# Performance work log

Hardware: AMD Instinct MI355X
Metric: run time of the kernel (lower is better)

The kernel has to match this reference:

```python
import jax, jax.numpy as jnp
import numpy as np

S1, S2, S3 = 2, 16, 1  # hardcoded layer sizes from __init__


def _lstm_cell(x, h, c, w_ih, w_hh, b_ih, b_hh):
    # torch.nn.LSTMCell gate order: i, f, g, o
    gates = x @ w_ih.T + b_ih + h @ w_hh.T + b_hh
    i, f, g, o = jnp.split(gates, 4, axis=-1)
    i = jax.nn.sigmoid(i)
    f = jax.nn.sigmoid(f)
    g = jnp.tanh(g)
    o = jax.nn.sigmoid(o)
    c_new = f * c + i * g
    h_new = o * jnp.tanh(c_new)
    return h_new, c_new


def setup_inputs() -> dict:
    key = jax.random.key(0)
    ks = jax.random.split(key, 16)
    B, T = 16384, 2048
    x = jax.random.normal(ks[0], (B, T * S1), dtype=jnp.float32)

    def u(k, shape, fan):
        bound = 1.0 / np.sqrt(fan)
        return jax.random.uniform(k, shape, jnp.float32, -bound, bound)

    return {
        "x": x,
        # lstm1: LSTMCell(2, 2)
        "w_ih1": u(ks[1], (4 * S1, S1), S1), "w_hh1": u(ks[2], (4 * S1, S1), S1),
        "b_ih1": u(ks[3], (4 * S1,), S1),   "b_hh1": u(ks[4], (4 * S1,), S1),
        # lstm2: LSTMCell(2, 16)
        "w_ih2": u(ks[5], (4 * S2, S1), S2), "w_hh2": u(ks[6], (4 * S2, S2), S2),
        "b_ih2": u(ks[7], (4 * S2,), S2),   "b_hh2": u(ks[8], (4 * S2,), S2),
        # lstm3: LSTMCell(16, 1)
        "w_ih3": u(ks[9], (4 * S3, S2), S3), "w_hh3": u(ks[10], (4 * S3, S3), S3),
        "b_ih3": u(ks[11], (4 * S3,), S3),  "b_hh3": u(ks[12], (4 * S3,), S3),
        # linear: Linear(1, 1)
        "w_lin": u(ks[13], (S3, S3), S3), "b_lin": u(ks[14], (S3,), S3),
    }


def reference(x, w_ih1, w_hh1, b_ih1, b_hh1,
              w_ih2, w_hh2, b_ih2, b_hh2,
              w_ih3, w_hh3, b_ih3, b_hh3,
              w_lin, b_lin):
    B = x.shape[0]
    T = x.shape[1] // S1
    # [B, T*2] -> [T, B, 2] (time-major for scan)
    xt = x.reshape(B, T, S1).transpose(1, 0, 2)

    h1 = jnp.zeros((B, S1), x.dtype); c1 = jnp.zeros((B, S1), x.dtype)
    h2 = jnp.zeros((B, S2), x.dtype); c2 = jnp.zeros((B, S2), x.dtype)
    h3 = jnp.zeros((B, S3), x.dtype); c3 = jnp.zeros((B, S3), x.dtype)

    def step(carry, x_t):
        h1, c1, h2, c2, h3, c3 = carry
        h1, c1 = _lstm_cell(x_t, h1, c1, w_ih1, w_hh1, b_ih1, b_hh1)
        h2, c2 = _lstm_cell(h1, h2, c2, w_ih2, w_hh2, b_ih2, b_hh2)
        h3, c3 = _lstm_cell(h2, h3, c3, w_ih3, w_hh3, b_ih3, b_hh3)
        out = h3 @ w_lin.T + b_lin  # [B, 1]
        return (h1, c1, h2, c2, h3, c3), out

    _, ys = jax.lax.scan(step, (h1, c1, h2, c2, h3, c3), xt)
    # ys: [T, B, 1] -> cat along dim=1 of per-step [B,1] outputs -> [B, T]
    return ys[:, :, 0].T
```

## Files before the change

### kernel.cpp

```cpp
#include <hip/hip_runtime.h>

typedef _Float16 f16x8 __attribute__((ext_vector_type(8)));
typedef float    f32x4 __attribute__((ext_vector_type(4)));
typedef unsigned u32x4 __attribute__((ext_vector_type(4)));

#define DEV __device__ __forceinline__

DEV float fexp2(float x){ return __builtin_amdgcn_exp2f(x); }
DEV float frcp (float x){ return __builtin_amdgcn_rcpf(x); }

DEV float sgm(float p){ return frcp(1.0f + fexp2(p)); }
DEV float tnc(float c){ return fmaf(2.f, sgm(c * -2.88539008177792682f), -1.f); }

DEV float shx(float v, int m){ return __shfl_xor(v, m, 64); }

DEV unsigned pkrne(float a, float b){
  unsigned short ha = __builtin_bit_cast(unsigned short, (_Float16)a);
  unsigned short hb = __builtin_bit_cast(unsigned short, (_Float16)b);
  return (unsigned)ha | ((unsigned)hb << 16);
}

#define L2E_N  (-1.44269504088896341f)
#define L2E2_N (-2.88539008177792682f)

__global__ __launch_bounds__(256, 1)
void lstm3_kernel(const float* __restrict__ x,
                  const float* __restrict__ w_ih1, const float* __restrict__ w_hh1,
                  const float* __restrict__ b_ih1, const float* __restrict__ b_hh1,
                  const float* __restrict__ w_ih2, const float* __restrict__ w_hh2,
                  const float* __restrict__ b_ih2, const float* __restrict__ b_hh2,
                  const float* __restrict__ w_ih3, const float* __restrict__ w_hh3,
                  const float* __restrict__ b_ih3, const float* __restrict__ b_hh3,
                  const float* __restrict__ w_lin, const float* __restrict__ b_lin,
                  float* __restrict__ out, int T)
{
  const int tid = threadIdx.x;
  const int l   = tid & 63;
  const int n   = l & 15;
  const int g   = l >> 4;
  const int wv  = tid >> 6;
  const int seq = 16 * (blockIdx.x * 4 + wv) + n;

  const int rA = g, rB = 4 + g;
  const float sAq = L2E_N;
  const float sBq = (g < 2) ? L2E2_N : L2E_N;
  const float m1  = (g < 2) ? 2.0f : 1.0f;
  const float a1  = (g < 2) ? -1.0f : 0.0f;
  const float w1ax = w_ih1[2*rA]*sAq,  w1ay = w_ih1[2*rA+1]*sAq;
  const float w1ah0 = w_hh1[2*rA]*sAq, w1ah1 = w_hh1[2*rA+1]*sAq;
  const float bbA  = (b_ih1[rA] + b_hh1[rA]) * sAq;
  const float w1bx = w_ih1[2*rB]*sBq,  w1by = w_ih1[2*rB+1]*sBq;
  const float w1bh0 = w_hh1[2*rB]*sBq, w1bh1 = w_hh1[2*rB+1]*sBq;
  const float bbB  = (b_ih1[rB] + b_hh1[rB]) * sBq;

  f16x8 af[4];
  f16x8 a2f[4];
  f32x4 cb[4];
  #pragma unroll
  for (int t = 0; t < 4; ++t){
    const float sc = (t == 2) ? L2E2_N : L2E_N;
    #pragma unroll
    for (int e = 0; e < 8; ++e){
      float v = 0.0f;
      if (e < 4) v = w_hh2[(16*t + n)*16 + (4*g + e)];
      af[t][e] = (_Float16)(v * sc);
      float v2 = 0.0f;
      if (g == 0 && e < 2) v2 = w_ih2[(16*t + n)*2 + e];
      a2f[t][e] = (_Float16)(v2 * sc);
    }
    #pragma unroll
    for (int j = 0; j < 4; ++j){
      const int r = 16*t + 4*g + j;
      cb[t][j] = (b_ih2[r] + b_hh2[r]) * sc;
    }
  }

  const float s3n = ((n & 3) == 2) ? L2E2_N : L2E_N;
  f16x8 a3f;
  #pragma unroll
  for (int e = 0; e < 8; ++e){
    float v = 0.0f;
    if (e < 4) v = w_ih3[16*(n & 3) + 4*g + e] * s3n;
    a3f[e] = (_Float16)v;
  }
  f32x4 c3v;
  float wh3s0, wh3s1, wh3s2, wh3s3;
  {
    const float s0 = L2E_N, s1 = L2E_N, s2 = L2E2_N, s3_ = L2E_N;
    c3v[0] = (b_ih3[0] + b_hh3[0]) * s0;
    c3v[1] = (b_ih3[1] + b_hh3[1]) * s1;
    c3v[2] = (b_ih3[2] + b_hh3[2]) * s2;
    c3v[3] = (b_ih3[3] + b_hh3[3]) * s3_;
    wh3s0 = w_hh3[0] * s0; wh3s1 = w_hh3[1] * s1;
    wh3s2 = w_hh3[2] * s2; wh3s3 = w_hh3[3] * s3_;
  }
  const float wl = w_lin[0], bl = b_lin[0];

  float c1 = 0.f, c3 = 0.f;
  float c2[4] = {0.f, 0.f, 0.f, 0.f};
  float h1a_all = 0.f, h1b_all = 0.f, h3 = 0.f;
  unsigned pAu = 0u, pBu = 0u;

  const float* xrow = x + (size_t)seq * (size_t)(2*T);
  float*       orow = out + (size_t)seq * (size_t)T;

  float4 pa = *(const float4*)(xrow);
  float4 pb = *(const float4*)(xrow + 4);

  float o0 = 0.f, o1 = 0.f, o2 = 0.f, o3 = 0.f;

  f32x4 dp0, dp1, dp2, dp3;
  {
    u32x4 bu; bu[0] = 0u; bu[1] = 0u; bu[2] = 0u; bu[3] = 0u;
    const f16x8 bv = __builtin_bit_cast(f16x8, bu);
    dp0 = __builtin_amdgcn_mfma_f32_16x16x32_f16(af[0], bv, cb[0], 0, 0, 0);
    dp1 = __builtin_amdgcn_mfma_f32_16x16x32_f16(af[1], bv, cb[1], 0, 0, 0);
    dp2 = __builtin_amdgcn_mfma_f32_16x16x32_f16(af[2], bv, cb[2], 0, 0, 0);
    dp3 = __builtin_amdgcn_mfma_f32_16x16x32_f16(af[3], bv, cb[3], 0, 0, 0);
  }

  const int NCH = T / 4;
  for (int ch = 0; ch < NCH; ++ch){
    const float4 ca = pa, cbv = pb;
    const int no = (ch + 1 < NCH) ? (ch + 1) * 8 : 0;
    pa = *(const float4*)(xrow + no);
    pb = *(const float4*)(xrow + no + 4);

    const bool cap = (g == (ch & 3));

    #pragma unroll
    for (int s = 0; s < 4; ++s){
      const float x0 = (s==0)?ca.x:(s==1)?ca.z:(s==2)?cbv.x:cbv.z;
      const float x1 = (s==0)?ca.y:(s==1)?ca.w:(s==2)?cbv.y:cbv.w;

      const float gA = fmaf(w1ax, x0, fmaf(w1ay, x1,
                       fmaf(w1ah0, h1a_all, fmaf(w1ah1, h1b_all, bbA))));
      const float gB = fmaf(w1bx, x0, fmaf(w1by, x1,
                       fmaf(w1bh0, h1a_all, fmaf(w1bh1, h1b_all, bbB))));
      const float zA = sgm(gA);
      const float zB = fmaf(sgm(gB), m1, a1);
      const float ig1 = zA * zB;
      const float fm = shx(zA, 32);
      c1 = fmaf(fm, c1, ig1);
      const float th1 = tnc(c1);
      const float om = shx(zB, 32);
      const float h1v = om * th1;
      const float t16 = shx(h1v, 16);
      const unsigned h1p = pkrne(h1v, t16);
      u32x4 b2u; b2u[0] = (g == 0) ? h1p : 0u; b2u[1] = 0u; b2u[2] = 0u; b2u[3] = 0u;
      const f16x8 b2v = __builtin_bit_cast(f16x8, b2u);
      const float a_c = (g & 1) ? t16 : h1v;
      const float b_c = (g & 1) ? h1v : t16;
      const float a32 = shx(a_c, 32);
      const float b32 = shx(b_c, 32);
      h1a_all = (g & 2) ? a32 : a_c;
      h1b_all = (g & 2) ? b32 : b_c;

      const f32x4 d0 = __builtin_amdgcn_mfma_f32_16x16x32_f16(a2f[0], b2v, dp0, 0, 0, 0);
      const f32x4 d1 = __builtin_amdgcn_mfma_f32_16x16x32_f16(a2f[1], b2v, dp1, 0, 0, 0);
      const f32x4 d2 = __builtin_amdgcn_mfma_f32_16x16x32_f16(a2f[2], b2v, dp2, 0, 0, 0);
      const f32x4 d3 = __builtin_amdgcn_mfma_f32_16x16x32_f16(a2f[3], b2v, dp3, 0, 0, 0);

      float h2l[4];
      #pragma unroll
      for (int j = 0; j < 4; ++j){
        const float ii = sgm(d0[j]);
        const float ff = sgm(d1[j]);
        const float gg = fmaf(2.f, sgm(d2[j]), -1.f);
        const float oo = sgm(d3[j]);
        c2[j] = fmaf(ff, c2[j], ii * gg);
        h2l[j] = oo * tnc(c2[j]);
      }
      pAu = pkrne(h2l[0], h2l[1]);
      pBu = pkrne(h2l[2], h2l[3]);

      u32x4 bu; bu[0] = pAu; bu[1] = pBu; bu[2] = 0u; bu[3] = 0u;
      const f16x8 bv = __builtin_bit_cast(f16x8, bu);
      dp0 = __builtin_amdgcn_mfma_f32_16x16x32_f16(af[0], bv, cb[0], 0, 0, 0);
      dp1 = __builtin_amdgcn_mfma_f32_16x16x32_f16(af[1], bv, cb[1], 0, 0, 0);
      dp2 = __builtin_amdgcn_mfma_f32_16x16x32_f16(af[2], bv, cb[2], 0, 0, 0);
      dp3 = __builtin_amdgcn_mfma_f32_16x16x32_f16(af[3], bv, cb[3], 0, 0, 0);

      const f32x4 d3v = __builtin_amdgcn_mfma_f32_16x16x32_f16(a3f, bv, c3v, 0, 0, 0);
      const float p_i = fmaf(wh3s0, h3, d3v[0]);
      const float p_f = fmaf(wh3s1, h3, d3v[1]);
      const float p_g = fmaf(wh3s2, h3, d3v[2]);
      const float p_o = fmaf(wh3s3, h3, d3v[3]);
      const float i3 = sgm(p_i);
      const float f3 = sgm(p_f);
      const float g3 = fmaf(2.f, sgm(p_g), -1.f);
      const float q3 = sgm(p_o);
      c3 = fmaf(f3, c3, i3 * g3);
      h3 = q3 * tnc(c3);
      const float yv = fmaf(wl, h3, bl);

      if      (s == 0) o0 = cap ? yv : o0;
      else if (s == 1) o1 = cap ? yv : o1;
      else if (s == 2) o2 = cap ? yv : o2;
      else             o3 = cap ? yv : o3;
    }

    if ((ch & 3) == 3){
      float4 o4; o4.x = o0; o4.y = o1; o4.z = o2; o4.w = o3;
      *(float4*)(orow + (ch >> 2) * 16 + 4 * g) = o4;
    }
  }
}

extern "C" void kernel_launch(void* const* d_in, const int* in_sizes, int n_in,
                              void* d_out, int out_size, void* d_ws, size_t ws_size,
                              hipStream_t stream)
{
  const float* x     = (const float*)d_in[0];
  const float* w_ih1 = (const float*)d_in[1];
  const float* w_hh1 = (const float*)d_in[2];
  const float* b_ih1 = (const float*)d_in[3];
  const float* b_hh1 = (const float*)d_in[4];
  const float* w_ih2 = (const float*)d_in[5];
  const float* w_hh2 = (const float*)d_in[6];
  const float* b_ih2 = (const float*)d_in[7];
  const float* b_hh2 = (const float*)d_in[8];
  const float* w_ih3 = (const float*)d_in[9];
  const float* w_hh3 = (const float*)d_in[10];
  const float* b_ih3 = (const float*)d_in[11];
  const float* b_hh3 = (const float*)d_in[12];
  const float* w_lin = (const float*)d_in[13];
  const float* b_lin = (const float*)d_in[14];
  float* out = (float*)d_out;

  const int T = 2048;
  const int B = in_sizes[0] / (2 * T);
  const int waves   = B / 16;
  const int blocks  = waves / 4;

  lstm3_kernel<<<blocks, 256, 0, stream>>>(
      x, w_ih1, w_hh1, b_ih1, b_hh1,
      w_ih2, w_hh2, b_ih2, b_hh2,
      w_ih3, w_hh3, b_ih3, b_hh3,
      w_lin, b_lin, out, T);
}
```

Measured before the change: 1.060 ms.

## Halve sequences per wave to double wave count and split per-lane transcendental work

Each wave now handles 8 sequences instead of 16, which doubles the number of waves. Lanes are remapped so every lane computes one layer-1 gate and two layer-2 hidden units instead of four, with cross-lane shuffles used to rebuild the shared operands. Launch bounds are raised to allow two blocks per CU. The aim is to cut the serial per-step transcendental latency per lane and add latency hiding. The cost is half-empty MFMA columns, extra shuffles, and twice the total MFMA work.

Result: slower. 1.380 ms (+30.1%).

```diff
diff --git a/kernel.cpp b/kernel.cpp
--- a/kernel.cpp
+++ b/kernel.cpp
@@ -13,6 +13,7 @@
 DEV float tnc(float c){ return fmaf(2.f, sgm(c * -2.88539008177792682f), -1.f); }
 
 DEV float shx(float v, int m){ return __shfl_xor(v, m, 64); }
+DEV unsigned shxu(unsigned v, int m){ return (unsigned)__shfl_xor((int)v, m, 64); }
 
 DEV unsigned pkrne(float a, float b){
   unsigned short ha = __builtin_bit_cast(unsigned short, (_Float16)a);
@@ -23,7 +24,7 @@
 #define L2E_N  (-1.44269504088896341f)
 #define L2E2_N (-2.88539008177792682f)
 
-__global__ __launch_bounds__(256, 1)
+__global__ __launch_bounds__(256, 2)
 void lstm3_kernel(const float* __restrict__ x,
                   const float* __restrict__ w_ih1, const float* __restrict__ w_hh1,
                   const float* __restrict__ b_ih1, const float* __restrict__ b_hh1,
@@ -36,25 +37,25 @@
 {
   const int tid = threadIdx.x;
   const int l   = tid & 63;
-  const int n   = l & 15;
-  const int g   = l >> 4;
+  const int n   = l & 7;
+  const int b8  = (l >> 3) & 1;
+  const int gp  = l >> 4;
+  const int col = l & 15;
+  const int kk  = (gp << 1) | b8;
   const int wv  = tid >> 6;
-  const int seq = 16 * (blockIdx.x * 4 + wv) + n;
-
-  const int rA = g, rB = 4 + g;
-  const float sAq = L2E_N;
-  const float sBq = (g < 2) ? L2E2_N : L2E_N;
-  const float m1  = (g < 2) ? 2.0f : 1.0f;
-  const float a1  = (g < 2) ? -1.0f : 0.0f;
-  const float w1ax = w_ih1[2*rA]*sAq,  w1ay = w_ih1[2*rA+1]*sAq;
-  const float w1ah0 = w_hh1[2*rA]*sAq, w1ah1 = w_hh1[2*rA+1]*sAq;
-  const float bbA  = (b_ih1[rA] + b_hh1[rA]) * sAq;
-  const float w1bx = w_ih1[2*rB]*sBq,  w1by = w_ih1[2*rB+1]*sBq;
-  const float w1bh0 = w_hh1[2*rB]*sBq, w1bh1 = w_hh1[2*rB+1]*sBq;
-  const float bbB  = (b_ih1[rB] + b_hh1[rB]) * sBq;
+  const int seq = 8 * (blockIdx.x * 4 + wv) + n;
+
+  const float sc1 = (kk == 4 || kk == 5) ? L2E2_N : L2E_N;
+  const float m1  = (kk == 4 || kk == 5) ? 2.0f : 1.0f;
+  const float a1v = (kk == 4 || kk == 5) ? -1.0f : 0.0f;
+  const float w1x0 = w_ih1[2*kk]   * sc1;
+  const float w1x1 = w_ih1[2*kk+1] * sc1;
+  const float w1h0 = w_hh1[2*kk]   * sc1;
+  const float w1h1 = w_hh1[2*kk+1] * sc1;
+  const float bb1  = (b_ih1[kk] + b_hh1[kk]) * sc1;
 
   f16x8 af[4];
-  f16x8 a2f[4];
+  unsigned a2p[4];
   f32x4 cb[4];
   #pragma unroll
   for (int t = 0; t < 4; ++t){
@@ -62,42 +63,40 @@
     #pragma unroll
     for (int e = 0; e < 8; ++e){
       float v = 0.0f;
-      if (e < 4) v = w_hh2[(16*t + n)*16 + (4*g + e)];
+      if (e < 4) v = w_hh2[(16*t + col)*16 + (4*gp + e)];
       af[t][e] = (_Float16)(v * sc);
-      float v2 = 0.0f;
-      if (g == 0 && e < 2) v2 = w_ih2[(16*t + n)*2 + e];
-      a2f[t][e] = (_Float16)(v2 * sc);
-    }
+    }
+    if (gp == 0)
+      a2p[t] = pkrne(w_ih2[(16*t + col)*2 + 0] * sc,
+                     w_ih2[(16*t + col)*2 + 1] * sc);
+    else
+      a2p[t] = 0u;
     #pragma unroll
     for (int j = 0; j < 4; ++j){
-      const int r = 16*t + 4*g + j;
+      const int r = 16*t + 4*gp + j;
       cb[t][j] = (b_ih2[r] + b_hh2[r]) * sc;
     }
   }
 
-  const float s3n = ((n & 3) == 2) ? L2E2_N : L2E_N;
+  const float s3n = ((col & 3) == 2) ? L2E2_N : L2E_N;
   f16x8 a3f;
   #pragma unroll
   for (int e = 0; e < 8; ++e){
     float v = 0.0f;
-    if (e < 4) v = w_ih3[16*(n & 3) + 4*g + e] * s3n;
+    if (e < 4) v = w_ih3[16*(col & 3) + 4*gp + e] * s3n;
     a3f[e] = (_Float16)v;
   }
   f32x4 c3v;
-  float wh3s0, wh3s1, wh3s2, wh3s3;
-  {
-    const float s0 = L2E_N, s1 = L2E_N, s2 = L2E2_N, s3_ = L2E_N;
-    c3v[0] = (b_ih3[0] + b_hh3[0]) * s0;
-    c3v[1] = (b_ih3[1] + b_hh3[1]) * s1;
-    c3v[2] = (b_ih3[2] + b_hh3[2]) * s2;
-    c3v[3] = (b_ih3[3] + b_hh3[3]) * s3_;
-    wh3s0 = w_hh3[0] * s0; wh3s1 = w_hh3[1] * s1;
-    wh3s2 = w_hh3[2] * s2; wh3s3 = w_hh3[3] * s3_;
-  }
+  c3v[0] = (b_ih3[0] + b_hh3[0]) * L2E_N;
+  c3v[1] = (b_ih3[1] + b_hh3[1]) * L2E_N;
+  c3v[2] = (b_ih3[2] + b_hh3[2]) * L2E2_N;
+  c3v[3] = (b_ih3[3] + b_hh3[3]) * L2E_N;
+  const float wh30 = w_hh3[0] * L2E_N,  wh31 = w_hh3[1] * L2E_N;
+  const float wh32 = w_hh3[2] * L2E2_N, wh33 = w_hh3[3] * L2E_N;
   const float wl = w_lin[0], bl = b_lin[0];
 
   float c1 = 0.f, c3 = 0.f;
-  float c2[4] = {0.f, 0.f, 0.f, 0.f};
+  float c2a = 0.f, c2b = 0.f;
   float h1a_all = 0.f, h1b_all = 0.f, h3 = 0.f;
   unsigned pAu = 0u, pBu = 0u;
 
@@ -126,53 +125,65 @@
     pa = *(const float4*)(xrow + no);
     pb = *(const float4*)(xrow + no + 4);
 
-    const bool cap = (g == (ch & 3));
+    const bool cap = (kk == (ch & 7));
 
     #pragma unroll
     for (int s = 0; s < 4; ++s){
       const float x0 = (s==0)?ca.x:(s==1)?ca.z:(s==2)?cbv.x:cbv.z;
       const float x1 = (s==0)?ca.y:(s==1)?ca.w:(s==2)?cbv.y:cbv.w;
 
-      const float gA = fmaf(w1ax, x0, fmaf(w1ay, x1,
-                       fmaf(w1ah0, h1a_all, fmaf(w1ah1, h1b_all, bbA))));
-      const float gB = fmaf(w1bx, x0, fmaf(w1by, x1,
-                       fmaf(w1bh0, h1a_all, fmaf(w1bh1, h1b_all, bbB))));
-      const float zA = sgm(gA);
-      const float zB = fmaf(sgm(gB), m1, a1);
-      const float ig1 = zA * zB;
-      const float fm = shx(zA, 32);
-      c1 = fmaf(fm, c1, ig1);
+      const float g1 = fmaf(w1x0, x0, fmaf(w1x1, x1,
+                       fmaf(w1h0, h1a_all, fmaf(w1h1, h1b_all, bb1))));
+      const float z1 = fmaf(sgm(g1), m1, a1v);
+      const float t1 = shx(z1, 32);
+      const float ig1 = z1 * t1;
+      const float u1 = shx(z1, 16);
+      const float v1 = shx(t1, 16);
+      const float fv = (gp & 2) ? v1 : u1;
+      const float ov = (gp & 2) ? u1 : v1;
+      c1 = fmaf(fv, c1, ig1);
       const float th1 = tnc(c1);
-      const float om = shx(zB, 32);
-      const float h1v = om * th1;
-      const float t16 = shx(h1v, 16);
-      const unsigned h1p = pkrne(h1v, t16);
-      u32x4 b2u; b2u[0] = (g == 0) ? h1p : 0u; b2u[1] = 0u; b2u[2] = 0u; b2u[3] = 0u;
+      const float hh = ov * th1;
+      const float t8 = shx(hh, 8);
+      const float ha0 = b8 ? t8 : hh;
+      const float hb0 = b8 ? hh : t8;
+      const float ua = shx(ha0, 16);
+      const float ub = shx(hb0, 16);
+      const float ha1 = (gp & 1) ? ua : ha0;
+      const float hb1 = (gp & 1) ? ub : hb0;
+      const float wa = shx(ha1, 32);
+      const float wb = shx(hb1, 32);
+      h1a_all = (gp & 2) ? wa : ha1;
+      h1b_all = (gp & 2) ? wb : hb1;
+      const unsigned h1p = pkrne(h1a_all, h1b_all);
+
+      u32x4 b2u; b2u[0] = (gp == 0) ? h1p : 0u; b2u[1] = 0u; b2u[2] = 0u; b2u[3] = 0u;
       const f16x8 b2v = __builtin_bit_cast(f16x8, b2u);
-      const float a_c = (g & 1) ? t16 : h1v;
-      const float b_c = (g & 1) ? h1v : t16;
-      const float a32 = shx(a_c, 32);
-      const float b32 = shx(b_c, 32);
-      h1a_all = (g & 2) ? a32 : a_c;
-      h1b_all = (g & 2) ? b32 : b_c;
-
-      const f32x4 d0 = __builtin_amdgcn_mfma_f32_16x16x32_f16(a2f[0], b2v, dp0, 0, 0, 0);
-      const f32x4 d1 = __builtin_amdgcn_mfma_f32_16x16x32_f16(a2f[1], b2v, dp1, 0, 0, 0);
-      const f32x4 d2 = __builtin_amdgcn_mfma_f32_16x16x32_f16(a2f[2], b2v, dp2, 0, 0, 0);
-      const f32x4 d3 = __builtin_amdgcn_mfma_f32_16x16x32_f16(a2f[3], b2v, dp3, 0, 0, 0);
-
-      float h2l[4];
-      #pragma unroll
-      for (int j = 0; j < 4; ++j){
-        const float ii = sgm(d0[j]);
-        const float ff = sgm(d1[j]);
-        const float gg = fmaf(2.f, sgm(d2[j]), -1.f);
-        const float oo = sgm(d3[j]);
-        c2[j] = fmaf(ff, c2[j], ii * gg);
-        h2l[j] = oo * tnc(c2[j]);
-      }
-      pAu = pkrne(h2l[0], h2l[1]);
-      pBu = pkrne(h2l[2], h2l[3]);
+      u32x4 a2u0; a2u0[0] = a2p[0]; a2u0[1] = 0u; a2u0[2] = 0u; a2u0[3] = 0u;
+      u32x4 a2u1; a2u1[0] = a2p[1]; a2u1[1] = 0u; a2u1[2] = 0u; a2u1[3] = 0u;
+      u32x4 a2u2; a2u2[0] = a2p[2]; a2u2[1] = 0u; a2u2[2] = 0u; a2u2[3] = 0u;
+      u32x4 a2u3; a2u3[0] = a2p[3]; a2u3[1] = 0u; a2u3[2] = 0u; a2u3[3] = 0u;
+      const f32x4 d0 = __builtin_amdgcn_mfma_f32_16x16x32_f16(__builtin_bit_cast(f16x8, a2u0), b2v, dp0, 0, 0, 0);
+      const f32x4 d1 = __builtin_amdgcn_mfma_f32_16x16x32_f16(__builtin_bit_cast(f16x8, a2u1), b2v, dp1, 0, 0, 0);
+      const f32x4 d2 = __builtin_amdgcn_mfma_f32_16x16x32_f16(__builtin_bit_cast(f16x8, a2u2), b2v, dp2, 0, 0, 0);
+      const f32x4 d3 = __builtin_amdgcn_mfma_f32_16x16x32_f16(__builtin_bit_cast(f16x8, a2u3), b2v, dp3, 0, 0, 0);
+
+      const float pAi = b8 ? d0[2] : d0[0], pBi = b8 ? d0[3] : d0[1];
+      const float pAf = b8 ? d1[2] : d1[0], pBf = b8 ? d1[3] : d1[1];
+      const float pAg = b8 ? d2[2] : d2[0], pBg = b8 ? d2[3] : d2[1];
+      const float pAo = b8 ? d3[2] : d3[0], pBo = b8 ? d3[3] : d3[1];
+      const float iA = sgm(pAi), fA = sgm(pAf), oA = sgm(pAo);
+      const float gA2 = fmaf(2.f, sgm(pAg), -1.f);
+      c2a = fmaf(fA, c2a, iA * gA2);
+      const float h2a = oA * tnc(c2a);
+      const float iB = sgm(pBi), fB = sgm(pBf), oB = sgm(pBo);
+      const float gB2 = fmaf(2.f, sgm(pBg), -1.f);
+      c2b = fmaf(fB, c2b, iB * gB2);
+      const float h2b = oB * tnc(c2b);
+      const unsigned pk  = pkrne(h2a, h2b);
+      const unsigned pko = shxu(pk, 8);
+      pAu = b8 ? pko : pk;
+      pBu = b8 ? pk : pko;
 
       u32x4 bu; bu[0] = pAu; bu[1] = pBu; bu[2] = 0u; bu[3] = 0u;
       const f16x8 bv = __builtin_bit_cast(f16x8, bu);
@@ -182,10 +193,10 @@
       dp3 = __builtin_amdgcn_mfma_f32_16x16x32_f16(af[3], bv, cb[3], 0, 0, 0);
 
       const f32x4 d3v = __builtin_amdgcn_mfma_f32_16x16x32_f16(a3f, bv, c3v, 0, 0, 0);
-      const float p_i = fmaf(wh3s0, h3, d3v[0]);
-      const float p_f = fmaf(wh3s1, h3, d3v[1]);
-      const float p_g = fmaf(wh3s2, h3, d3v[2]);
-      const float p_o = fmaf(wh3s3, h3, d3v[3]);
+      const float p_i = fmaf(wh30, h3, d3v[0]);
+      const float p_f = fmaf(wh31, h3, d3v[1]);
+      const float p_g = fmaf(wh32, h3, d3v[2]);
+      const float p_o = fmaf(wh33, h3, d3v[3]);
       const float i3 = sgm(p_i);
       const float f3 = sgm(p_f);
       const float g3 = fmaf(2.f, sgm(p_g), -1.f);
@@ -200,9 +211,9 @@
       else             o3 = cap ? yv : o3;
     }
 
-    if ((ch & 3) == 3){
+    if ((ch & 7) == 7){
       float4 o4; o4.x = o0; o4.y = o1; o4.z = o2; o4.w = o3;
-      *(float4*)(orow + (ch >> 2) * 16 + 4 * g) = o4;
+      *(float4*)(orow + (ch >> 3) * 32 + 4 * kk) = o4;
     }
   }
 }
@@ -230,7 +241,7 @@
 
   const int T = 2048;
   const int B = in_sizes[0] / (2 * T);
-  const int waves   = B / 16;
+  const int waves   = B / 8;
   const int blocks  = waves / 4;
 
   lstm3_kernel<<<blocks, 256, 0, stream>>>(
```

## Software-pipeline layer-1 LSTM one step ahead of layer-2 MFMA

Applied to the files above, without the earlier changes.

Layer 1 is now computed one timestep ahead: the layer-2 MFMAs for step t use the h1 value computed in the previous iteration, and layer 1 for step t+1 runs after those MFMAs are issued. Its scalar exp/rcp/shuffle chain can then overlap the MFMA latency instead of sitting in front of it. Input loading changes from float4 prefetch per 4-step chunk to a per-step float2 prefetch two steps ahead, with the index clamped at the end. This adds a per-step load with more address arithmetic and extends h1 register lifetime.

Result: slower. 1.085 ms (+2.4%).

```diff
diff --git a/kernel.cpp b/kernel.cpp
--- a/kernel.cpp
+++ b/kernel.cpp
@@ -84,28 +84,51 @@
     a3f[e] = (_Float16)v;
   }
   f32x4 c3v;
-  float wh3s0, wh3s1, wh3s2, wh3s3;
-  {
-    const float s0 = L2E_N, s1 = L2E_N, s2 = L2E2_N, s3_ = L2E_N;
-    c3v[0] = (b_ih3[0] + b_hh3[0]) * s0;
-    c3v[1] = (b_ih3[1] + b_hh3[1]) * s1;
-    c3v[2] = (b_ih3[2] + b_hh3[2]) * s2;
-    c3v[3] = (b_ih3[3] + b_hh3[3]) * s3_;
-    wh3s0 = w_hh3[0] * s0; wh3s1 = w_hh3[1] * s1;
-    wh3s2 = w_hh3[2] * s2; wh3s3 = w_hh3[3] * s3_;
-  }
+  c3v[0] = (b_ih3[0] + b_hh3[0]) * L2E_N;
+  c3v[1] = (b_ih3[1] + b_hh3[1]) * L2E_N;
+  c3v[2] = (b_ih3[2] + b_hh3[2]) * L2E2_N;
+  c3v[3] = (b_ih3[3] + b_hh3[3]) * L2E_N;
+  const float wh30 = w_hh3[0] * L2E_N,  wh31 = w_hh3[1] * L2E_N;
+  const float wh32 = w_hh3[2] * L2E2_N, wh33 = w_hh3[3] * L2E_N;
   const float wl = w_lin[0], bl = b_lin[0];
 
   float c1 = 0.f, c3 = 0.f;
   float c2[4] = {0.f, 0.f, 0.f, 0.f};
   float h1a_all = 0.f, h1b_all = 0.f, h3 = 0.f;
   unsigned pAu = 0u, pBu = 0u;
+  unsigned h1p = 0u;
 
   const float* xrow = x + (size_t)seq * (size_t)(2*T);
   float*       orow = out + (size_t)seq * (size_t)T;
 
-  float4 pa = *(const float4*)(xrow);
-  float4 pb = *(const float4*)(xrow + 4);
+  float2 x_use = *(const float2*)(xrow);
+  float2 x_pre = *(const float2*)(xrow + 2);
+
+  #define LSTM1_STEP(X0, X1)                                                   \
+  {                                                                            \
+    const float gA = fmaf(w1ax, (X0), fmaf(w1ay, (X1),                         \
+                     fmaf(w1ah0, h1a_all, fmaf(w1ah1, h1b_all, bbA))));        \
+    const float gB = fmaf(w1bx, (X0), fmaf(w1by, (X1),                         \
+                     fmaf(w1bh0, h1a_all, fmaf(w1bh1, h1b_all, bbB))));        \
+    const float zA = sgm(gA);                                                  \
+    const float zB = fmaf(sgm(gB), m1, a1);                                    \
+    const float ig1 = zA * zB;                                                 \
+    const float fm = shx(zA, 32);                                              \
+    c1 = fmaf(fm, c1, ig1);                                                    \
+    const float th1 = tnc(c1);                                                 \
+    const float om = shx(zB, 32);                                              \
+    const float h1v = om * th1;                                                \
+    const float t16 = shx(h1v, 16);                                            \
+    h1p = pkrne(h1v, t16);                         \
+    const float a_c = (g & 1) ? t16 : h1v;                                     \
+    const float b_c = (g & 1) ? h1v : t16;                                     \
+    const float a32 = shx(a_c, 32);                                            \
+    const float b32 = shx(b_c, 32);                                            \
+    h1a_all = (g & 2) ? a32 : a_c;                                             \
+    h1b_all = (g & 2) ? b32 : b_c;                                             \
+  }
+
+  LSTM1_STEP(x_use.x, x_use.y)
 
   float o0 = 0.f, o1 = 0.f, o2 = 0.f, o3 = 0.f;
 
@@ -121,45 +144,23 @@
 
   const int NCH = T / 4;
   for (int ch = 0; ch < NCH; ++ch){
-    const float4 ca = pa, cbv = pb;
-    const int no = (ch + 1 < NCH) ? (ch + 1) * 8 : 0;
-    pa = *(const float4*)(xrow + no);
-    pb = *(const float4*)(xrow + no + 4);
-
     const bool cap = (g == (ch & 3));
 
     #pragma unroll
     for (int s = 0; s < 4; ++s){
-      const float x0 = (s==0)?ca.x:(s==1)?ca.z:(s==2)?cbv.x:cbv.z;
-      const float x1 = (s==0)?ca.y:(s==1)?ca.w:(s==2)?cbv.y:cbv.w;
-
-      const float gA = fmaf(w1ax, x0, fmaf(w1ay, x1,
-                       fmaf(w1ah0, h1a_all, fmaf(w1ah1, h1b_all, bbA))));
-      const float gB = fmaf(w1bx, x0, fmaf(w1by, x1,
-                       fmaf(w1bh0, h1a_all, fmaf(w1bh1, h1b_all, bbB))));
-      const float zA = sgm(gA);
-      const float zB = fmaf(sgm(gB), m1, a1);
-      const float ig1 = zA * zB;
-      const float fm = shx(zA, 32);
-      c1 = fmaf(fm, c1, ig1);
-      const float th1 = tnc(c1);
-      const float om = shx(zB, 32);
-      const float h1v = om * th1;
-      const float t16 = shx(h1v, 16);
-      const unsigned h1p = pkrne(h1v, t16);
       u32x4 b2u; b2u[0] = (g == 0) ? h1p : 0u; b2u[1] = 0u; b2u[2] = 0u; b2u[3] = 0u;
       const f16x8 b2v = __builtin_bit_cast(f16x8, b2u);
-      const float a_c = (g & 1) ? t16 : h1v;
-      const float b_c = (g & 1) ? h1v : t16;
-      const float a32 = shx(a_c, 32);
-      const float b32 = shx(b_c, 32);
-      h1a_all = (g & 2) ? a32 : a_c;
-      h1b_all = (g & 2) ? b32 : b_c;
-
       const f32x4 d0 = __builtin_amdgcn_mfma_f32_16x16x32_f16(a2f[0], b2v, dp0, 0, 0, 0);
       const f32x4 d1 = __builtin_amdgcn_mfma_f32_16x16x32_f16(a2f[1], b2v, dp1, 0, 0, 0);
       const f32x4 d2 = __builtin_amdgcn_mfma_f32_16x16x32_f16(a2f[2], b2v, dp2, 0, 0, 0);
       const f32x4 d3 = __builtin_amdgcn_mfma_f32_16x16x32_f16(a2f[3], b2v, dp3, 0, 0, 0);
+
+      const float2 xv = x_pre;
+      const int ti = 4*ch + s + 2;
+      const int tc = (ti < T) ? ti : (T - 1);
+      x_pre = *(const float2*)(xrow + 2*tc);
+
+      LSTM1_STEP(xv.x, xv.y)
 
       float h2l[4];
       #pragma unroll
@@ -182,10 +183,10 @@
       dp3 = __builtin_amdgcn_mfma_f32_16x16x32_f16(af[3], bv, cb[3], 0, 0, 0);
 
       const f32x4 d3v = __builtin_amdgcn_mfma_f32_16x16x32_f16(a3f, bv, c3v, 0, 0, 0);
-      const float p_i = fmaf(wh3s0, h3, d3v[0]);
-      const float p_f = fmaf(wh3s1, h3, d3v[1]);
-      const float p_g = fmaf(wh3s2, h3, d3v[2]);
-      const float p_o = fmaf(wh3s3, h3, d3v[3]);
+      const float p_i = fmaf(wh30, h3, d3v[0]);
+      const float p_f = fmaf(wh31, h3, d3v[1]);
+      const float p_g = fmaf(wh32, h3, d3v[2]);
+      const float p_o = fmaf(wh33, h3, d3v[3]);
       const float i3 = sgm(p_i);
       const float f3 = sgm(p_f);
       const float g3 = fmaf(2.f, sgm(p_g), -1.f);
@@ -205,6 +206,7 @@
       *(float4*)(orow + (ch >> 2) * 16 + 4 * g) = o4;
     }
   }
+  #undef LSTM1_STEP
 }
 
 extern "C" void kernel_launch(void* const* d_in, const int* in_sizes, int n_in,
```
